# Optimization experiments

Hardware: AMD Instinct MI355X
Metric: run time of the kernel (lower is better)

## Reference

```python
import jax, jax.numpy as jnp
import numpy as np

B, T = 1024, 320
EEG_CH, GEO_CH, F1, HID, OUT = 64, 18, 8, 32, 4
THETA0, BETA, TAU_A = 0.5, 1.8, 0.36
EPS = 1e-5


def _bn(x, s, b, m, v):
    # eval-mode BatchNorm with running stats (flax default eps 1e-5)
    return (x - m) * jax.lax.rsqrt(v + EPS) * s + b


def _dwconv(x, w, b, groups):
    # depthwise temporal conv, x: (B, T, C), w: (K, 1, C*F1), SAME padding
    y = jax.lax.conv_general_dilated(x, w, (1,), 'SAME', dimension_numbers=('NWC', 'WIO', 'NWC'), feature_group_count=groups)
    return y + b


def _spike(x):
    return jnp.where(x >= 0.0, 1.0, 0.0)


def _forward(x_eeg, x_geo, eeg_conv_w, eeg_conv_b, eeg_bn1_s, eeg_bn1_b, eeg_bn1_m, eeg_bn1_v, eeg_dense_w, eeg_dense_b, eeg_bn2_s, eeg_bn2_b, eeg_bn2_m, eeg_bn2_v, geo_conv_w, geo_conv_b, geo_bn1_s, geo_bn1_b, geo_bn1_m, geo_bn1_v, geo_dense_w, geo_dense_b, geo_bn2_s, geo_bn2_b, geo_bn2_m, geo_bn2_v, gamma, fc1_w, fc1_b, fc2_w, fc2_b):
    Bc = x_eeg.shape[0]
    xe = _bn(_dwconv(x_eeg, eeg_conv_w, eeg_conv_b, EEG_CH), eeg_bn1_s, eeg_bn1_b, eeg_bn1_m, eeg_bn1_v)
    xe = _bn(xe @ eeg_dense_w + eeg_dense_b, eeg_bn2_s, eeg_bn2_b, eeg_bn2_m, eeg_bn2_v)
    eeg_enc = jax.nn.relu(xe)                      # (B, T, HID)
    xg = _bn(_dwconv(x_geo, geo_conv_w, geo_conv_b, GEO_CH), geo_bn1_s, geo_bn1_b, geo_bn1_m, geo_bn1_v)
    xg = _bn(xg @ geo_dense_w + geo_dense_b, geo_bn2_s, geo_bn2_b, geo_bn2_m, geo_bn2_v)
    geo_mod = jax.nn.sigmoid(xg)                   # (B, T, HID)

    def step(carry, inp):
        m1, m2, m3, ma, eta, mli, prev = carry
        ce, cg = inp
        m1 = 0.9 * m1 + ce; s1 = _spike(m1 - 0.7); m1 = m1 * (1.0 - s1)
        m2 = 0.8 * m2 + ce; s2 = _spike(m2 - 0.5); m2 = m2 * (1.0 - s2)
        m3 = 0.6 * m3 + ce; s3 = _spike(m3 - 0.3); m3 = m3 * (1.0 - s3)
        hr = (s1 + s2 + s3) / 3.0
        eta = TAU_A * eta + (1.0 - TAU_A) * prev
        theta = THETA0 + BETA * eta - gamma * cg
        ma = 0.8 * ma + hr
        sa = _spike(ma - theta)
        ma = ma * (1.0 - sa)
        mli = 0.9 * mli + sa
        return (m1, m2, m3, ma, eta, mli, sa), mli

    z = jnp.zeros((Bc, HID), x_eeg.dtype)
    _, seq = jax.lax.scan(step, (z, z, z, z, z, z, z), (jnp.swapaxes(eeg_enc, 0, 1), jnp.swapaxes(geo_mod, 0, 1)))
    seq = jnp.transpose(seq, (1, 2, 0))            # (B, HID, T)
    win = seq.reshape(Bc, HID, 10, 32)
    dp = (jnp.mean(win[..., 16:], -1) - jnp.mean(win[..., :16], -1)).reshape(Bc, HID * 10)
    return jax.nn.elu(dp @ fc1_w + fc1_b) @ fc2_w + fc2_b


def setup_inputs() -> dict:
    ks = iter(jax.random.split(jax.random.key(0), 48))
    def rn(shape, s=1.0):
        return jax.random.normal(next(ks), shape, jnp.float32) * s
    ECH, GCH = EEG_CH * F1, GEO_CH * F1
    return {
        'x_eeg': rn((B, T, EEG_CH)),
        'x_geo': rn((B, T, GEO_CH)),
        'eeg_conv_w': rn((32, 1, ECH), 0.05), 'eeg_conv_b': jnp.zeros((ECH,), jnp.float32),
        'eeg_bn1_s': 1.0 + rn((ECH,), 0.1), 'eeg_bn1_b': rn((ECH,), 0.1),
        'eeg_bn1_m': rn((ECH,), 0.1), 'eeg_bn1_v': 1.0 + 0.1 * jax.random.uniform(next(ks), (ECH,), jnp.float32),
        'eeg_dense_w': rn((ECH, HID), 0.05), 'eeg_dense_b': jnp.zeros((HID,), jnp.float32),
        'eeg_bn2_s': 1.0 + rn((HID,), 0.1), 'eeg_bn2_b': rn((HID,), 0.1),
        'eeg_bn2_m': rn((HID,), 0.1), 'eeg_bn2_v': 1.0 + 0.1 * jax.random.uniform(next(ks), (HID,), jnp.float32),
        'geo_conv_w': rn((32, 1, GCH), 0.05), 'geo_conv_b': jnp.zeros((GCH,), jnp.float32),
        'geo_bn1_s': 1.0 + rn((GCH,), 0.1), 'geo_bn1_b': rn((GCH,), 0.1),
        'geo_bn1_m': rn((GCH,), 0.1), 'geo_bn1_v': 1.0 + 0.1 * jax.random.uniform(next(ks), (GCH,), jnp.float32),
        'geo_dense_w': rn((GCH, HID), 0.05), 'geo_dense_b': jnp.zeros((HID,), jnp.float32),
        'geo_bn2_s': 1.0 + rn((HID,), 0.1), 'geo_bn2_b': rn((HID,), 0.1),
        'geo_bn2_m': rn((HID,), 0.1), 'geo_bn2_v': 1.0 + 0.1 * jax.random.uniform(next(ks), (HID,), jnp.float32),
        'gamma': jnp.full((HID,), 0.5, jnp.float32),
        'fc1_w': rn((HID * 10, 128), 0.05), 'fc1_b': jnp.zeros((128,), jnp.float32),
        'fc2_w': rn((128, OUT), 0.05), 'fc2_b': jnp.zeros((OUT,), jnp.float32),
    }


def reference(x_eeg, x_geo, eeg_conv_w, eeg_conv_b, eeg_bn1_s, eeg_bn1_b, eeg_bn1_m, eeg_bn1_v, eeg_dense_w, eeg_dense_b, eeg_bn2_s, eeg_bn2_b, eeg_bn2_m, eeg_bn2_v, geo_conv_w, geo_conv_b, geo_bn1_s, geo_bn1_b, geo_bn1_m, geo_bn1_v, geo_dense_w, geo_dense_b, geo_bn2_s, geo_bn2_b, geo_bn2_m, geo_bn2_v, gamma, fc1_w, fc1_b, fc2_w, fc2_b):
    return _forward(x_eeg, x_geo, eeg_conv_w, eeg_conv_b, eeg_bn1_s, eeg_bn1_b, eeg_bn1_m, eeg_bn1_v, eeg_dense_w, eeg_dense_b, eeg_bn2_s, eeg_bn2_b, eeg_bn2_m, eeg_bn2_v, geo_conv_w, geo_conv_b, geo_bn1_s, geo_bn1_b, geo_bn1_m, geo_bn1_v, geo_dense_w, geo_dense_b, geo_bn2_s, geo_bn2_b, geo_bn2_m, geo_bn2_v, gamma, fc1_w, fc1_b, fc2_w, fc2_b)
```

## Files before the change

kernel.cpp:

```cpp
#include <hip/hip_runtime.h>
#include <hip/hip_bf16.h>
#include <math.h>

#define BSZ   1024
#define TLEN  320
#define EEGC  64
#define GEOC  18
#define ECH   512
#define GCH   144
#define HID   32
#define KW    32
#define TT    32
#define NT    (TLEN/TT)

#define OFF_ENC  0
#define OFF_MOD  (OFF_ENC + BSZ*TLEN*HID)
#define OFF_DP   (OFF_MOD + BSZ*TLEN*HID)
#define OFF_CWE  (OFF_DP + BSZ*HID*10)
#define OFF_CWG  (OFF_CWE + ECH*KW)
#define OFF_DWE  (OFF_CWG + GCH*KW)
#define OFF_DWG  (OFF_DWE + ECH*HID)
#define OFF_BTE  (OFF_DWG + GCH*HID)
#define OFF_BTG  (OFF_BTE + HID)
#define OFF_GAM  (OFF_BTG + HID)

struct P29 { const float* p[29]; };

__global__ __launch_bounds__(256) void prep_kernel(P29 P, float* __restrict__ ws)
{
    __shared__ float pse[8][32];
    __shared__ float psg[8][32];
    const int tid = threadIdx.x;
    const int gid = blockIdx.x * 256 + tid;
    const int gstride = 33 * 256;
    float* convW_e = ws + OFF_CWE;
    float* convW_g = ws + OFF_CWG;
    float* dW_e    = ws + OFF_DWE;
    float* dW_g    = ws + OFF_DWG;

    for (int i = gid; i < ECH * KW; i += gstride) {
        int c = i >> 5, k = i & 31;
        float A1 = P.p[2][c] * rsqrtf(P.p[5][c] + 1e-5f);
        convW_e[c * KW + k] = P.p[0][(size_t)k * ECH + c] * A1;
    }
    for (int i = gid; i < GCH * KW; i += gstride) {
        int c = i >> 5, k = i & 31;
        float A1 = P.p[14][c] * rsqrtf(P.p[17][c] + 1e-5f);
        convW_g[c * KW + k] = P.p[12][(size_t)k * GCH + c] * A1;
    }
    for (int i = gid; i < ECH * HID; i += gstride) {
        int h = i & 31;
        float A2 = P.p[8][h] * rsqrtf(P.p[11][h] + 1e-5f);
        dW_e[i] = P.p[6][i] * A2;
    }
    for (int i = gid; i < GCH * HID; i += gstride) {
        int h = i & 31;
        float A2 = P.p[20][h] * rsqrtf(P.p[23][h] + 1e-5f);
        dW_g[i] = P.p[18][i] * A2;
    }
    for (int i = gid; i < HID; i += gstride) ws[OFF_GAM + i] = P.p[24][i];

    if (blockIdx.x == 0) {
        {
            const int h = tid & 31, part = tid >> 5;
            float s = 0.f;
            for (int c = part * 64; c < part * 64 + 64; ++c) {
                float A1 = P.p[2][c] * rsqrtf(P.p[5][c] + 1e-5f);
                float C1 = (P.p[1][c] - P.p[4][c]) * A1 + P.p[3][c];
                s += C1 * P.p[6][(size_t)c * HID + h];
            }
            pse[part][h] = s;
            float sg = 0.f;
            for (int c = part * 18; c < part * 18 + 18; ++c) {
                float A1 = P.p[14][c] * rsqrtf(P.p[17][c] + 1e-5f);
                float C1 = (P.p[13][c] - P.p[16][c]) * A1 + P.p[15][c];
                sg += C1 * P.p[18][(size_t)c * HID + h];
            }
            psg[part][h] = sg;
        }
        __syncthreads();
        if (tid < HID) {
            int h = tid;
            float A2 = P.p[8][h] * rsqrtf(P.p[11][h] + 1e-5f);
            float s = pse[0][h] + pse[1][h] + pse[2][h] + pse[3][h]
                    + pse[4][h] + pse[5][h] + pse[6][h] + pse[7][h];
            ws[OFF_BTE + h] = A2 * (s + P.p[7][h] - P.p[10][h]) + P.p[9][h];
        } else if (tid >= 64 && tid < 64 + HID) {
            int h = tid - 64;
            float A2 = P.p[20][h] * rsqrtf(P.p[23][h] + 1e-5f);
            float s = psg[0][h] + psg[1][h] + psg[2][h] + psg[3][h]
                    + psg[4][h] + psg[5][h] + psg[6][h] + psg[7][h];
            ws[OFF_BTG + h] = A2 * (s + P.p[19][h] - P.p[22][h]) + P.p[21][h];
        }
    }
}

__device__ __forceinline__ void conv_stream(const float4* __restrict__ xp4,
                                            const float* __restrict__ w,
                                            float* __restrict__ acc)
{
    float4 cur = xp4[0];
    #pragma unroll
    for (int j4 = 0; j4 < 12; ++j4) {
        float4 nxt = (j4 < 11) ? xp4[j4 + 1] : cur;
        #pragma unroll
        for (int i2 = 0; i2 < 4; ++i2) {
            const int i = j4 * 4 + i2;
            const float xv = (i2 == 0) ? cur.x : (i2 == 1) ? cur.y
                           : (i2 == 2) ? cur.z : cur.w;
            const int tlo = (i - 31 > 0) ? (i - 31) : 0;
            const int thi = (i < 15) ? i : 15;
            #pragma unroll
            for (int t = tlo; t <= thi; ++t)
                acc[t] = fmaf(xv, w[i - t], acc[t]);
        }
        cur = nxt;
    }
}

__device__ __forceinline__ void geo_conv_unit(const float* __restrict__ convW,
                                              const float* __restrict__ xsT,
                                              float* __restrict__ cz,
                                              int c, int th)
{
    float w[KW];
    const float4* wp4 = (const float4*)(convW + c * KW);
    #pragma unroll
    for (int k4 = 0; k4 < 8; ++k4) {
        float4 v = wp4[k4];
        w[4*k4+0]=v.x; w[4*k4+1]=v.y; w[4*k4+2]=v.z; w[4*k4+3]=v.w;
    }
    float acc[16];
    #pragma unroll
    for (int t = 0; t < 16; ++t) acc[t] = 0.f;
    conv_stream((const float4*)(xsT + (c >> 3) * 68 + th * 16), w, acc);
    float4* czp = (float4*)(cz + c * 36 + th * 16);
    czp[0] = make_float4(acc[0],  acc[1],  acc[2],  acc[3]);
    czp[1] = make_float4(acc[4],  acc[5],  acc[6],  acc[7]);
    czp[2] = make_float4(acc[8],  acc[9],  acc[10], acc[11]);
    czp[3] = make_float4(acc[12], acc[13], acc[14], acc[15]);
}

__global__ __launch_bounds__(256)
void path_both(const float* __restrict__ xe, const float* __restrict__ xg,
               float* __restrict__ ws)
{
    __shared__ __align__(16) float smem[6408];

    const int b   = blockIdx.y;
    const int tid = threadIdx.x;

    if (blockIdx.x < NT) {
        const int t0 = blockIdx.x * TT;
        float* xsT = smem;
        float* cz  = smem + 1088;
        const float* convW = ws + OFF_CWE;
        const float* dW    = ws + OFF_DWE;
        float* enc         = ws + OFF_ENC;

        const float* xb = xe + (size_t)b * (TLEN * EEGC);

        const int tg = tid & 7, hg = (tid >> 3) & 7, q = tid >> 6;
        const int c_loc = tid & 127, th = tid >> 7;
        float a00=0,a01=0,a02=0,a03=0, a10=0,a11=0,a12=0,a13=0;
        float a20=0,a21=0,a22=0,a23=0, a30=0,a31=0,a32=0,a33=0;

        #pragma unroll 1
        for (int ph = 0; ph < 4; ++ph) {
            if (ph) __syncthreads();
            if (tid < 252) {
                const int sj = tid >> 2, sc4 = tid & 3;
                const int st = t0 - 15 + sj;
                float4 sv = make_float4(0.f, 0.f, 0.f, 0.f);
                if (st >= 0 && st < TLEN)
                    sv = *(const float4*)(xb + (size_t)st * EEGC + ph * 16 + sc4 * 4);
                float* p = &xsT[(sc4 * 4) * 68 + sj];
                p[0] = sv.x; p[68] = sv.y; p[136] = sv.z; p[204] = sv.w;
            }
            __syncthreads();
            {
                const int c   = ph * 128 + c_loc;
                const int chl = c_loc >> 3;
                float w[KW];
                const float4* wp4 = (const float4*)(convW + c * KW);
                #pragma unroll
                for (int k4 = 0; k4 < 8; ++k4) {
                    float4 v = wp4[k4];
                    w[4*k4+0]=v.x; w[4*k4+1]=v.y; w[4*k4+2]=v.z; w[4*k4+3]=v.w;
                }
                float acc[16];
                #pragma unroll
                for (int t = 0; t < 16; ++t) acc[t] = 0.f;
                conv_stream((const float4*)(&xsT[chl * 68 + th * 16]), w, acc);
                float4* czp = (float4*)(cz + c_loc * 36 + th * 16);
                czp[0] = make_float4(acc[0],  acc[1],  acc[2],  acc[3]);
                czp[1] = make_float4(acc[4],  acc[5],  acc[6],  acc[7]);
                czp[2] = make_float4(acc[8],  acc[9],  acc[10], acc[11]);
                czp[3] = make_float4(acc[12], acc[13], acc[14], acc[15]);
            }
            __syncthreads();
            {
                const float* dWh = dW + (size_t)(ph * 128 + q * 32) * HID + hg * 4;
                const float* czb = cz + (q * 32) * 36 + tg * 4;
                float4 wvb[4], cvb[2];
                wvb[0] = *(const float4*)(dWh + 0 * HID);
                wvb[1] = *(const float4*)(dWh + 1 * HID);
                wvb[2] = *(const float4*)(dWh + 2 * HID);
                wvb[3] = *(const float4*)(dWh + 3 * HID);
                cvb[0] = *(const float4*)(czb + 0 * 36);
                cvb[1] = *(const float4*)(czb + 1 * 36);
                #pragma unroll
                for (int ci = 0; ci < 32; ++ci) {
                    float4 cv = cvb[ci & 1];
                    float4 wv = wvb[ci & 3];
                    if (ci + 2 < 32) cvb[ci & 1] = *(const float4*)(czb + (ci + 2) * 36);
                    if (ci + 4 < 32) wvb[ci & 3] = *(const float4*)(dWh + (ci + 4) * HID);
                    a00 = fmaf(cv.x, wv.x, a00); a01 = fmaf(cv.x, wv.y, a01);
                    a02 = fmaf(cv.x, wv.z, a02); a03 = fmaf(cv.x, wv.w, a03);
                    a10 = fmaf(cv.y, wv.x, a10); a11 = fmaf(cv.y, wv.y, a11);
                    a12 = fmaf(cv.y, wv.z, a12); a13 = fmaf(cv.y, wv.w, a13);
                    a20 = fmaf(cv.z, wv.x, a20); a21 = fmaf(cv.z, wv.y, a21);
                    a22 = fmaf(cv.z, wv.z, a22); a23 = fmaf(cv.z, wv.w, a23);
                    a30 = fmaf(cv.w, wv.x, a30); a31 = fmaf(cv.w, wv.y, a31);
                    a32 = fmaf(cv.w, wv.z, a32); a33 = fmaf(cv.w, wv.w, a33);
                }
            }
        }

        __syncthreads();
        float* stash = cz;
        {
            const int s = (tid >> 1) & 3;
            float4* sp = (float4*)(stash + tid * 16);
            sp[s ^ 0] = make_float4(a00,a01,a02,a03);
            sp[s ^ 1] = make_float4(a10,a11,a12,a13);
            sp[s ^ 2] = make_float4(a20,a21,a22,a23);
            sp[s ^ 3] = make_float4(a30,a31,a32,a33);
        }
        __syncthreads();
        {
            const int t = tid >> 3, hq = tid & 7;
            const int pg = (t & 3) ^ (t >> 3);
            float4 v = make_float4(0.f,0.f,0.f,0.f);
            #pragma unroll
            for (int qq = 0; qq < 4; ++qq) {
                const int partner = qq * 64 + hq * 8 + (t >> 2);
                float4 s = *(const float4*)(stash + partner * 16 + pg * 4);
                v.x += s.x; v.y += s.y; v.z += s.z; v.w += s.w;
            }
            float4 bias = *(const float4*)(ws + OFF_BTE + hq * 4);
            v.x = fmaxf(v.x + bias.x, 0.f);
            v.y = fmaxf(v.y + bias.y, 0.f);
            v.z = fmaxf(v.z + bias.z, 0.f);
            v.w = fmaxf(v.w + bias.w, 0.f);
            *(float4*)(enc + ((size_t)(b * TLEN + t0 + t)) * HID + hq * 4) = v;
        }
    } else {
        const int t0 = (blockIdx.x - NT) * TT;
        float* xsT = smem;
        float* cz  = smem + 1224;
        const float* convW = ws + OFF_CWG;
        const float* dW    = ws + OFF_DWG;
        float* mod         = ws + OFF_MOD;

        const float* xb = xg + (size_t)b * (TLEN * GEOC);
        for (int i = tid; i < 63 * GEOC; i += 256) {
            int j = i / GEOC, ch = i - j * GEOC;
            int t = t0 - 15 + j;
            xsT[ch * 68 + j] = (t >= 0 && t < TLEN) ? xb[(size_t)t * GEOC + ch] : 0.f;
        }
        __syncthreads();

        geo_conv_unit(convW, xsT, cz, tid >> 1, tid & 1);
        if (tid < 32)
            geo_conv_unit(convW, xsT, cz, 128 + (tid >> 1), tid & 1);
        __syncthreads();

        const int tg = tid & 7, hg = (tid >> 3) & 7, q = tid >> 6;
        float a00=0,a01=0,a02=0,a03=0, a10=0,a11=0,a12=0,a13=0;
        float a20=0,a21=0,a22=0,a23=0, a30=0,a31=0,a32=0,a33=0;
        {
            const float* dWh = dW + (size_t)(q * 36) * HID + hg * 4;
            const float* czb = cz + (q * 36) * 36 + tg * 4;
            #pragma unroll 2
            for (int ci = 0; ci < 36; ++ci) {
                float4 cv = *(const float4*)(czb + ci * 36);
                float4 wv = *(const float4*)(dWh + ci * HID);
                a00 = fmaf(cv.x, wv.x, a00); a01 = fmaf(cv.x, wv.y, a01);
                a02 = fmaf(cv.x, wv.z, a02); a03 = fmaf(cv.x, wv.w, a03);
                a10 = fmaf(cv.y, wv.x, a10); a11 = fmaf(cv.y, wv.y, a11);
                a12 = fmaf(cv.y, wv.z, a12); a13 = fmaf(cv.y, wv.w, a13);
                a20 = fmaf(cv.z, wv.x, a20); a21 = fmaf(cv.z, wv.y, a21);
                a22 = fmaf(cv.z, wv.z, a22); a23 = fmaf(cv.z, wv.w, a23);
                a30 = fmaf(cv.w, wv.x, a30); a31 = fmaf(cv.w, wv.y, a31);
                a32 = fmaf(cv.w, wv.z, a32); a33 = fmaf(cv.w, wv.w, a33);
            }
        }
        __syncthreads();
        float* stash = cz;
        {
            float4* sp = (float4*)(stash + tid * 20);
            sp[0] = make_float4(a00,a01,a02,a03);
            sp[1] = make_float4(a10,a11,a12,a13);
            sp[2] = make_float4(a20,a21,a22,a23);
            sp[3] = make_float4(a30,a31,a32,a33);
        }
        __syncthreads();
        {
            const int t = tid >> 3, hq = tid & 7;
            float4 v = make_float4(0.f,0.f,0.f,0.f);
            #pragma unroll
            for (int qq = 0; qq < 4; ++qq) {
                const int partner = qq * 64 + hq * 8 + (t >> 2);
                float4 s = *(const float4*)(stash + partner * 20 + (t & 3) * 4);
                v.x += s.x; v.y += s.y; v.z += s.z; v.w += s.w;
            }
            float4 bias = *(const float4*)(ws + OFF_BTG + hq * 4);
            v.x = 1.f / (1.f + expf(-(v.x + bias.x)));
            v.y = 1.f / (1.f + expf(-(v.y + bias.y)));
            v.z = 1.f / (1.f + expf(-(v.z + bias.z)));
            v.w = 1.f / (1.f + expf(-(v.w + bias.w)));
            *(float4*)(mod + ((size_t)(b * TLEN + t0 + t)) * HID + hq * 4) = v;
        }
    }
}

#define SSTEP(CE, CG) { \
    const float ce = (CE), cg = (CG); \
    m1 = 0.9f * m1 + ce; float s1 = ((m1 - 0.7f) >= 0.f) ? 1.f : 0.f; m1 = m1 * (1.f - s1); \
    m2 = 0.8f * m2 + ce; float s2 = ((m2 - 0.5f) >= 0.f) ? 1.f : 0.f; m2 = m2 * (1.f - s2); \
    m3 = 0.6f * m3 + ce; float s3 = ((m3 - 0.3f) >= 0.f) ? 1.f : 0.f; m3 = m3 * (1.f - s3); \
    const float hr = (s1 + s2 + s3) / 3.0f; \
    eta = 0.36f * eta + 0.64f * prev; \
    const float theta = 0.5f + 1.8f * eta - g * cg; \
    ma = 0.8f * ma + hr; \
    const float sa = ((ma - theta) >= 0.f) ? 1.f : 0.f; \
    ma = ma * (1.f - sa); \
    mli = 0.9f * mli + sa; \
    prev = sa; }

__global__ __launch_bounds__(128) void scan_head_kernel(
    float* __restrict__ ws,
    const float* __restrict__ f1w, const float* __restrict__ f1b,
    const float* __restrict__ f2w, const float* __restrict__ f2b,
    float* __restrict__ out)
{
    __shared__ __align__(16) float dps[4][320];
    __shared__ float act[4][128];
    const int tid = threadIdx.x;
    const int grp = tid >> 5, h = tid & 31;
    const int b = blockIdx.x * 4 + grp;

    {
        const float g = ws[OFF_GAM + h];
        const float* pe = ws + OFF_ENC + (size_t)b * TLEN * HID + h;
        const float* pg = ws + OFF_MOD + (size_t)b * TLEN * HID + h;
        float* dpp = &dps[grp][h * 10];

        float m1 = 0.f, m2 = 0.f, m3 = 0.f, ma = 0.f, eta = 0.f, mli = 0.f, prev = 0.f;
        float acc_lo = 0.f, acc_hi = 0.f;
        float ceA[16], cgA[16], ceB[16], cgB[16];

        #pragma unroll
        for (int i = 0; i < 16; ++i) { ceA[i] = pe[i * HID]; cgA[i] = pg[i * HID]; }

        #pragma unroll 1
        for (int ch = 0; ch < 20; ch += 2) {
            const int baseB = (ch + 1) * 16;
            #pragma unroll
            for (int i = 0; i < 16; ++i) {
                ceB[i] = pe[(baseB + i) * HID];
                cgB[i] = pg[(baseB + i) * HID];
            }
            #pragma unroll
            for (int i = 0; i < 16; ++i) {
                SSTEP(ceA[i], cgA[i]);
                acc_lo += mli;
            }
            if (ch + 2 < 20) {
                const int baseA = (ch + 2) * 16;
                #pragma unroll
                for (int i = 0; i < 16; ++i) {
                    ceA[i] = pe[(baseA + i) * HID];
                    cgA[i] = pg[(baseA + i) * HID];
                }
            }
            #pragma unroll
            for (int i = 0; i < 16; ++i) {
                SSTEP(ceB[i], cgB[i]);
                acc_hi += mli;
            }
            dpp[ch >> 1] = acc_hi * (1.f / 16.f) - acc_lo * (1.f / 16.f);
            acc_lo = 0.f; acc_hi = 0.f;
        }
    }
    __syncthreads();

    {
        const int j = tid;
        #pragma unroll 1
        for (int gb = 0; gb < 4; ++gb) {
            const float* dpb = dps[gb];
            float a0 = 0.f, a1 = 0.f, a2 = 0.f, a3 = 0.f;
            #pragma unroll 4
            for (int i = 0; i < 320; i += 4) {
                a0 = fmaf(dpb[i + 0], f1w[(i + 0) * 128 + j], a0);
                a1 = fmaf(dpb[i + 1], f1w[(i + 1) * 128 + j], a1);
                a2 = fmaf(dpb[i + 2], f1w[(i + 2) * 128 + j], a2);
                a3 = fmaf(dpb[i + 3], f1w[(i + 3) * 128 + j], a3);
            }
            float a = f1b[j] + ((a0 + a1) + (a2 + a3));
            act[gb][j] = (a > 0.f) ? a : expm1f(a);
        }
    }
    __syncthreads();

    if (tid < 16) {
        const int gb = tid >> 2, j = tid & 3;
        float o = f2b[j];
        for (int jj = 0; jj < 128; ++jj)
            o = fmaf(act[gb][jj], f2w[jj * 4 + j], o);
        out[(blockIdx.x * 4 + gb) * 4 + j] = o;
    }
}

extern "C" void kernel_launch(void* const* d_in, const int* in_sizes, int n_in,
                              void* d_out, int out_size, void* d_ws, size_t ws_size,
                              hipStream_t stream)
{
    float* ws = (float*)d_ws;

    P29 P;
    for (int k = 0; k < 29; ++k) P.p[k] = (const float*)d_in[k + 2];
    prep_kernel<<<33, 256, 0, stream>>>(P, ws);

    path_both<<<dim3(2 * NT, BSZ), 256, 0, stream>>>(
        (const float*)d_in[0], (const float*)d_in[1], ws);

    scan_head_kernel<<<BSZ / 4, 128, 0, stream>>>(
        ws, (const float*)d_in[27], (const float*)d_in[28],
        (const float*)d_in[29], (const float*)d_in[30], (float*)d_out);
}
```

Baseline: 690.1 us.

## Prefetch next EEG channel slab during dense stage and register-pipeline geo dense loop

The EEG encoder loop now loads the first input slab before the phase loop. For each later phase, it issues the global load for the next channel slab into registers before the dense accumulation and writes it to shared memory afterward, so global latency overlaps with FMA work. The stash for the cross-thread reduction moves to the start of shared memory. The geo dense loop gets the same rotating register prefetch of weights and conv outputs already used on the EEG side. This costs extra live registers and a larger unrolled loop, which may lower occupancy.

After: 1.107 ms. 60.4% more time.

```diff
diff --git a/kernel.cpp b/kernel.cpp
--- a/kernel.cpp
+++ b/kernel.cpp
@@ -165,19 +165,19 @@
         float a00=0,a01=0,a02=0,a03=0, a10=0,a11=0,a12=0,a13=0;
         float a20=0,a21=0,a22=0,a23=0, a30=0,a31=0,a32=0,a33=0;
 
+        if (tid < 252) {
+            const int sj = tid >> 2, sc4 = tid & 3;
+            const int st = t0 - 15 + sj;
+            float4 sv = make_float4(0.f, 0.f, 0.f, 0.f);
+            if (st >= 0 && st < TLEN)
+                sv = *(const float4*)(xb + (size_t)st * EEGC + sc4 * 4);
+            float* p = &xsT[(sc4 * 4) * 68 + sj];
+            p[0] = sv.x; p[68] = sv.y; p[136] = sv.z; p[204] = sv.w;
+        }
+        __syncthreads();
+
         #pragma unroll 1
         for (int ph = 0; ph < 4; ++ph) {
-            if (ph) __syncthreads();
-            if (tid < 252) {
-                const int sj = tid >> 2, sc4 = tid & 3;
-                const int st = t0 - 15 + sj;
-                float4 sv = make_float4(0.f, 0.f, 0.f, 0.f);
-                if (st >= 0 && st < TLEN)
-                    sv = *(const float4*)(xb + (size_t)st * EEGC + ph * 16 + sc4 * 4);
-                float* p = &xsT[(sc4 * 4) * 68 + sj];
-                p[0] = sv.x; p[68] = sv.y; p[136] = sv.z; p[204] = sv.w;
-            }
-            __syncthreads();
             {
                 const int c   = ph * 128 + c_loc;
                 const int chl = c_loc >> 3;
@@ -199,6 +199,15 @@
                 czp[3] = make_float4(acc[12], acc[13], acc[14], acc[15]);
             }
             __syncthreads();
+
+            float4 sv = make_float4(0.f, 0.f, 0.f, 0.f);
+            if (ph < 3 && tid < 252) {
+                const int sj = tid >> 2, sc4 = tid & 3;
+                const int st = t0 - 15 + sj;
+                if (st >= 0 && st < TLEN)
+                    sv = *(const float4*)(xb + (size_t)st * EEGC + (ph + 1) * 16 + sc4 * 4);
+            }
+
             {
                 const float* dWh = dW + (size_t)(ph * 128 + q * 32) * HID + hg * 4;
                 const float* czb = cz + (q * 32) * 36 + tg * 4;
@@ -225,10 +234,17 @@
                     a32 = fmaf(cv.w, wv.z, a32); a33 = fmaf(cv.w, wv.w, a33);
                 }
             }
-        }
-
-        __syncthreads();
-        float* stash = cz;
+
+            if (ph < 3 && tid < 252) {
+                const int sj = tid >> 2, sc4 = tid & 3;
+                float* p = &xsT[(sc4 * 4) * 68 + sj];
+                p[0] = sv.x; p[68] = sv.y; p[136] = sv.z; p[204] = sv.w;
+            }
+            __syncthreads();
+        }
+
+        float* stash = cz - 1088 + 1088;
+        stash = smem;
         {
             const int s = (tid >> 1) & 3;
             float4* sp = (float4*)(stash + tid * 16);
@@ -282,10 +298,19 @@
         {
             const float* dWh = dW + (size_t)(q * 36) * HID + hg * 4;
             const float* czb = cz + (q * 36) * 36 + tg * 4;
-            #pragma unroll 2
+            float4 wvb[4], cvb[2];
+            wvb[0] = *(const float4*)(dWh + 0 * HID);
+            wvb[1] = *(const float4*)(dWh + 1 * HID);
+            wvb[2] = *(const float4*)(dWh + 2 * HID);
+            wvb[3] = *(const float4*)(dWh + 3 * HID);
+            cvb[0] = *(const float4*)(czb + 0 * 36);
+            cvb[1] = *(const float4*)(czb + 1 * 36);
+            #pragma unroll
             for (int ci = 0; ci < 36; ++ci) {
-                float4 cv = *(const float4*)(czb + ci * 36);
-                float4 wv = *(const float4*)(dWh + ci * HID);
+                float4 cv = cvb[ci & 1];
+                float4 wv = wvb[ci & 3];
+                if (ci + 2 < 36) cvb[ci & 1] = *(const float4*)(czb + (ci + 2) * 36);
+                if (ci + 4 < 36) wvb[ci & 3] = *(const float4*)(dWh + (ci + 4) * HID);
                 a00 = fmaf(cv.x, wv.x, a00); a01 = fmaf(cv.x, wv.y, a01);
                 a02 = fmaf(cv.x, wv.z, a02); a03 = fmaf(cv.x, wv.w, a03);
                 a10 = fmaf(cv.y, wv.x, a10); a11 = fmaf(cv.y, wv.y, a11);
```
